# Kernel optimization log

Measured on AMD Instinct MI355X. Metric: run time of the kernel, lower is better.

The kernel has to match this reference:

```python
import jax, jax.numpy as jnp
import numpy as np

N_NODES = 20000
N_EDGES = 640000
B = 256
GNN_DIM = 256
HID = 512
INNER = 2048
RANK = 512
N_CLASSES = 3
N_GENES = 6640


def _ln(x, s, b, eps=1e-5):
    mu = jnp.mean(x, axis=-1, keepdims=True)
    var = jnp.mean(jnp.square(x - mu), axis=-1, keepdims=True)
    return (x - mu) * jax.lax.rsqrt(var + eps) * s + b


def setup_inputs() -> dict:
    key = jax.random.key(0)
    ks = jax.random.split(key, 16)
    s = 0.02
    return {
        "node_indices": jax.random.randint(ks[0], (B,), 0, N_NODES, dtype=jnp.int32),
        "edge_index": jax.random.randint(ks[1], (2, N_EDGES), 0, N_NODES, dtype=jnp.int32),
        "edge_weight": jax.random.uniform(ks[2], (N_EDGES,), dtype=jnp.float32),
        "partial_emb": jax.random.normal(ks[3], (N_NODES, GNN_DIM), dtype=jnp.float32),
        "oov_emb": jnp.zeros((1, GNN_DIM), jnp.float32),
        "gnn_ln_s": jnp.ones((3, GNN_DIM), jnp.float32),
        "gnn_ln_b": jnp.zeros((3, GNN_DIM), jnp.float32),
        "gnn_w": jax.random.normal(ks[4], (3, GNN_DIM, GNN_DIM), jnp.float32) * s,
        "gnn_b": jnp.zeros((3, GNN_DIM), jnp.float32),
        "post_w": jax.random.normal(ks[5], (GNN_DIM, GNN_DIM), jnp.float32) * s,
        "post_b": jnp.zeros((GNN_DIM,), jnp.float32),
        "pin_w": jax.random.normal(ks[6], (GNN_DIM, HID), jnp.float32) * s,
        "pin_b": jnp.zeros((HID,), jnp.float32),
        "blk_ln_s": jnp.ones((6, HID), jnp.float32),
        "blk_ln_b": jnp.zeros((6, HID), jnp.float32),
        "blk_w1": jax.random.normal(ks[7], (6, HID, INNER), jnp.float32) * s,
        "blk_b1": jnp.zeros((6, INNER), jnp.float32),
        "blk_w2": jax.random.normal(ks[8], (6, INNER, HID), jnp.float32) * s,
        "blk_b2": jnp.zeros((6, HID), jnp.float32),
        "pout_w": jax.random.normal(ks[9], (HID, N_CLASSES * RANK), jnp.float32) * s,
        "pout_b": jnp.zeros((N_CLASSES * RANK,), jnp.float32),
        "out_gene_emb": jax.random.normal(ks[10], (N_GENES, RANK), jnp.float32) * s,
    }


def reference(node_indices, edge_index, edge_weight, partial_emb, oov_emb,
              gnn_ln_s, gnn_ln_b, gnn_w, gnn_b, post_w, post_b,
              pin_w, pin_b, blk_ln_s, blk_ln_b, blk_w1, blk_b1, blk_w2, blk_b2,
              pout_w, pout_b, out_gene_emb):
    n = partial_emb.shape[0]
    src, dst = edge_index[0], edge_index[1]
    # --- trainable GNN tail: 3 layers of (LN -> weighted scatter-sum -> Linear -> ReLU) + residual ---
    x = partial_emb
    for i in range(3):
        h = _ln(x, gnn_ln_s[i], gnn_ln_b[i])
        msg = h[src] * edge_weight[:, None]              # [E, 256] gather (memory-bound)
        agg = jax.ops.segment_sum(msg, dst, num_segments=n)
        h = jax.nn.relu(agg @ gnn_w[i] + gnn_b[i])
        x = h + x
    x = x @ post_w + post_b                              # post_mp
    # --- OOV-safe perturbation embedding lookup ---
    oov = node_indices < 0
    safe = jnp.where(oov, 0, node_indices)
    pert = jnp.where(oov[:, None], oov_emb, x[safe])     # [B, 256]
    # --- bilinear head ---
    h = pert @ pin_w + pin_b
    for i in range(6):
        z = _ln(h, blk_ln_s[i], blk_ln_b[i])
        z = jax.nn.gelu(z @ blk_w1[i] + blk_b1[i], approximate=False)
        h = h + z @ blk_w2[i] + blk_b2[i]                # dropout = identity (eval)
    proj = (h @ pout_w + pout_b).reshape(h.shape[0], N_CLASSES, RANK)
    logits = jnp.einsum('bcr,gr->bcg', proj, out_gene_emb)
    return logits
```

## Files before the change

### kernel.cpp

```cpp
#include <hip/hip_runtime.h>
#include <hip/hip_bf16.h>
#include <math.h>

#define NNODES 20000
#define NEDGES 640000
#define BSZ 256
#define GDIM 256
#define HID 512
#define INNER 2048
#define RANK 512
#define NCLS 3
#define NGENES 6640

typedef __attribute__((ext_vector_type(8))) short bf16x8;
typedef __attribute__((ext_vector_type(4))) float f32x4;
typedef __attribute__((ext_vector_type(4))) unsigned u32x4;

__device__ inline float bf2f(unsigned short u) {
    return __uint_as_float(((unsigned)u) << 16);
}
__device__ inline unsigned short f2bf(float f) {
    unsigned u = __float_as_uint(f);
    u = u + 0x7fff + ((u >> 16) & 1);
    return (unsigned short)(u >> 16);
}
__device__ inline unsigned pk2(float a, float b) {
    return (unsigned)f2bf(a) | ((unsigned)f2bf(b) << 16);
}

__device__ inline u32x4 ld16_cg(const void* p) {
    u32x4 r;
    asm volatile("global_load_dwordx4 %0, %1, off sc0 sc1" : "=v"(r) : "v"(p) : "memory");
    return r;
}
__device__ inline void st4f_cg(void* p, float v) {
    asm volatile("global_store_dword %0, %1, off sc0 sc1" :: "v"(p), "v"(v) : "memory");
}
__device__ inline void st2_cg(void* p, unsigned short v) {
    unsigned w = v;
    asm volatile("global_store_short %0, %1, off sc0 sc1" :: "v"(p), "v"(w) : "memory");
}
__device__ inline void waitvm0(void) {
    asm volatile("s_waitcnt vmcnt(0)" ::: "memory");
    __builtin_amdgcn_sched_barrier(0);
}

__global__ void hist_k(const int* __restrict__ dst, int* __restrict__ counts, int E) {
    int e = blockIdx.x * 256 + threadIdx.x;
    if (e < E) atomicAdd(&counts[dst[e]], 1);
}

__global__ void scan1_k(const int* __restrict__ counts, int* __restrict__ incl,
                        int* __restrict__ bsums, int n) {
    __shared__ int s[256];
    int i = blockIdx.x * 256 + threadIdx.x;
    int v = (i < n) ? counts[i] : 0;
    s[threadIdx.x] = v;
    __syncthreads();
    for (int off = 1; off < 256; off <<= 1) {
        int t = (threadIdx.x >= off) ? s[threadIdx.x - off] : 0;
        __syncthreads();
        s[threadIdx.x] += t;
        __syncthreads();
    }
    if (i < n) incl[i] = s[threadIdx.x];
    if (threadIdx.x == 255) bsums[blockIdx.x] = s[255];
}

__global__ void scan2_k(const int* __restrict__ bsums, int* __restrict__ boffs, int nb) {
    __shared__ int s[128];
    int tid = threadIdx.x;
    int v = (tid < nb) ? bsums[tid] : 0;
    s[tid] = v;
    __syncthreads();
    for (int off = 1; off < 128; off <<= 1) {
        int t = (tid >= off) ? s[tid - off] : 0;
        __syncthreads();
        s[tid] += t;
        __syncthreads();
    }
    if (tid < nb) boffs[tid] = s[tid] - v;
}

__global__ void scan3_k(const int* __restrict__ incl, const int* __restrict__ counts,
                        const int* __restrict__ boffs, int* __restrict__ row_start,
                        int* __restrict__ cursor, int n) {
    int i = blockIdx.x * 256 + threadIdx.x;
    if (i < n) {
        int st = incl[i] - counts[i] + boffs[blockIdx.x];
        row_start[i] = st;
        cursor[i] = st;
    }
}

__global__ void scatter_k(const int* __restrict__ src, const int* __restrict__ dst,
                          const float* __restrict__ w, int* __restrict__ cursor,
                          int2* __restrict__ ep, int E) {
    int e = blockIdx.x * 256 + threadIdx.x;
    if (e < E) {
        int d = dst[e];
        int p = atomicAdd(&cursor[d], 1);
        ep[p] = make_int2(src[e], __float_as_int(w[e]));
    }
}

__global__ void flag_k(const int* __restrict__ idx, const int* __restrict__ row_start,
                       const int* __restrict__ counts, const int2* __restrict__ ep,
                       int* __restrict__ flag) {
    int r4 = blockIdx.x * 4 + (threadIdx.x >> 6);
    int lane = threadIdx.x & 63;
    int id = idx[r4];
    int row = id < 0 ? 0 : id;
    if (lane == 0) flag[row] = 1;
    int beg = row_start[row], cnt = counts[row];
    for (int t = lane; t < cnt; t += 64) flag[ep[beg + t].x] = 1;
}

__global__ void convall_k(const float* __restrict__ gnn_w, const float* __restrict__ post_w,
                          const float* __restrict__ pin_w, const float* __restrict__ blk_w1,
                          const float* __restrict__ blk_w2, const float* __restrict__ pout_w,
                          const float* __restrict__ gene, unsigned short* __restrict__ gnnT,
                          unsigned short* __restrict__ postT, unsigned short* __restrict__ pinT,
                          unsigned short* __restrict__ w1T, unsigned short* __restrict__ w2T,
                          unsigned short* __restrict__ poutT,
                          unsigned short* __restrict__ geneb) {
    int b = blockIdx.x;
    if (b >= 13440) {
        int t = b - 13440;
        const float4* xp = (const float4*)gene;
        int i = t * 512 + threadIdx.x * 2;
        float4 a = xp[i], c = xp[i + 1];
        *(ushort4*)(geneb + (size_t)i * 4) =
            make_ushort4(f2bf(a.x), f2bf(a.y), f2bf(a.z), f2bf(a.w));
        *(ushort4*)(geneb + (size_t)i * 4 + 4) =
            make_ushort4(f2bf(c.x), f2bf(c.y), f2bf(c.z), f2bf(c.w));
        return;
    }
    const float* W;
    unsigned short* WT;
    int K, N, tile;
    if (b < 192) {
        int l = b >> 6;
        tile = b & 63;
        W = gnn_w + (size_t)l * GDIM * GDIM;
        WT = gnnT + (size_t)l * GDIM * GDIM;
        K = GDIM; N = GDIM;
    } else if (b < 256) {
        tile = b - 192; W = post_w; WT = postT; K = GDIM; N = GDIM;
    } else if (b < 384) {
        tile = b - 256; W = pin_w; WT = pinT; K = GDIM; N = HID;
    } else if (b < 6528) {
        int t = b - 384;
        int l = t >> 10;
        tile = t & 1023;
        W = blk_w1 + (size_t)l * HID * INNER;
        WT = w1T + (size_t)l * INNER * HID;
        K = HID; N = INNER;
    } else if (b < 12672) {
        int t = b - 6528;
        int l = t >> 10;
        tile = t & 1023;
        W = blk_w2 + (size_t)l * INNER * HID;
        WT = w2T + (size_t)l * HID * INNER;
        K = INNER; N = HID;
    } else {
        tile = b - 12672; W = pout_w; WT = poutT; K = HID; N = NCLS * RANK;
    }
    __shared__ float s[32][33];
    int ntx = N >> 5;
    int k0 = (tile / ntx) << 5;
    int n0 = (tile % ntx) << 5;
    int tx = threadIdx.x & 31, ty = threadIdx.x >> 5;
#pragma unroll
    for (int i = 0; i < 4; i++)
        s[ty + 8 * i][tx] = W[(size_t)(k0 + ty + 8 * i) * N + n0 + tx];
    __syncthreads();
#pragma unroll
    for (int i = 0; i < 4; i++)
        WT[(size_t)(n0 + ty + 8 * i) * K + k0 + tx] = f2bf(s[tx][ty + 8 * i]);
}

template <bool FLAGGED>
__global__ void lnb_k(const float* __restrict__ X, const float* __restrict__ sc,
                      const float* __restrict__ bi, unsigned short* __restrict__ Y, int M,
                      const int* __restrict__ flag) {
    int row = blockIdx.x * 4 + (threadIdx.x >> 6);
    int lane = threadIdx.x & 63;
    if (row >= M) return;
    if (FLAGGED && !flag[row]) return;
    float4 v = ((const float4*)(X + (size_t)row * GDIM))[lane];
    float sum = v.x + v.y + v.z + v.w;
#pragma unroll
    for (int off = 32; off >= 1; off >>= 1) sum += __shfl_xor(sum, off);
    float mu = sum / GDIM;
    float a = v.x - mu, b = v.y - mu, c = v.z - mu, d = v.w - mu;
    float sq = a * a + b * b + c * c + d * d;
#pragma unroll
    for (int off = 32; off >= 1; off >>= 1) sq += __shfl_xor(sq, off);
    float rstd = rsqrtf(sq / GDIM + 1e-5f);
    float4 s4 = ((const float4*)sc)[lane];
    float4 b4 = ((const float4*)bi)[lane];
    *(ushort4*)(Y + (size_t)row * GDIM + lane * 4) =
        make_ushort4(f2bf(a * rstd * s4.x + b4.x), f2bf(b * rstd * s4.y + b4.y),
                     f2bf(c * rstd * s4.z + b4.z), f2bf(d * rstd * s4.w + b4.w));
}

__device__ inline void agg_row(int beg, int cnt, int lane, const int2* __restrict__ ep,
                               const unsigned short* __restrict__ H, float& a0, float& a1,
                               float& a2, float& a3) {
    int t = 0;
    for (; t + 16 <= cnt; t += 16) {
        int2 e[16];
#pragma unroll
        for (int u = 0; u < 16; u++) e[u] = ep[beg + t + u];
        ushort4 v[16];
#pragma unroll
        for (int u = 0; u < 16; u++)
            v[u] = *(const ushort4*)(H + (size_t)e[u].x * GDIM + lane * 4);
#pragma unroll
        for (int u = 0; u < 16; u++) {
            float w = __int_as_float(e[u].y);
            a0 = fmaf(bf2f(v[u].x), w, a0);
            a1 = fmaf(bf2f(v[u].y), w, a1);
            a2 = fmaf(bf2f(v[u].z), w, a2);
            a3 = fmaf(bf2f(v[u].w), w, a3);
        }
    }
    for (; t + 4 <= cnt; t += 4) {
        int2 e[4];
#pragma unroll
        for (int u = 0; u < 4; u++) e[u] = ep[beg + t + u];
        ushort4 v[4];
#pragma unroll
        for (int u = 0; u < 4; u++)
            v[u] = *(const ushort4*)(H + (size_t)e[u].x * GDIM + lane * 4);
#pragma unroll
        for (int u = 0; u < 4; u++) {
            float w = __int_as_float(e[u].y);
            a0 = fmaf(bf2f(v[u].x), w, a0);
            a1 = fmaf(bf2f(v[u].y), w, a1);
            a2 = fmaf(bf2f(v[u].z), w, a2);
            a3 = fmaf(bf2f(v[u].w), w, a3);
        }
    }
    for (; t < cnt; t++) {
        int2 e = ep[beg + t];
        float w = __int_as_float(e.y);
        ushort4 v = *(const ushort4*)(H + (size_t)e.x * GDIM + lane * 4);
        a0 = fmaf(bf2f(v.x), w, a0);
        a1 = fmaf(bf2f(v.y), w, a1);
        a2 = fmaf(bf2f(v.z), w, a2);
        a3 = fmaf(bf2f(v.w), w, a3);
    }
}

template <bool FLAGGED>
__global__ void aggb_k(const int* __restrict__ row_start, const int* __restrict__ counts,
                       const int2* __restrict__ ep, const unsigned short* __restrict__ H,
                       unsigned short* __restrict__ AGG, int n, const int* __restrict__ flag) {
    int row = blockIdx.x * 4 + (threadIdx.x >> 6);
    int lane = threadIdx.x & 63;
    if (row >= n) return;
    if (FLAGGED && !flag[row]) return;
    float a0 = 0.f, a1 = 0.f, a2 = 0.f, a3 = 0.f;
    agg_row(row_start[row], counts[row], lane, ep, H, a0, a1, a2, a3);
    *(ushort4*)(AGG + (size_t)row * GDIM + lane * 4) =
        make_ushort4(f2bf(a0), f2bf(a1), f2bf(a2), f2bf(a3));
}

__global__ void aggsel_k(const int* __restrict__ idx, const int* __restrict__ row_start,
                         const int* __restrict__ counts, const int2* __restrict__ ep,
                         const unsigned short* __restrict__ H, unsigned short* __restrict__ AGG) {
    int b = blockIdx.x * 4 + (threadIdx.x >> 6);
    int lane = threadIdx.x & 63;
    int id = idx[b];
    int row = id < 0 ? 0 : id;
    float a0 = 0.f, a1 = 0.f, a2 = 0.f, a3 = 0.f;
    agg_row(row_start[row], counts[row], lane, ep, H, a0, a1, a2, a3);
    *(ushort4*)(AGG + (size_t)b * GDIM + lane * 4) =
        make_ushort4(f2bf(a0), f2bf(a1), f2bf(a2), f2bf(a3));
}

template <int ACT, bool RES, bool BIAS>
__global__ __launch_bounds__(256) void mgemm_k(const unsigned short* __restrict__ A,
                                               const unsigned short* __restrict__ BT,
                                               const float* __restrict__ bias,
                                               const float* __restrict__ R,
                                               float* __restrict__ C, int M, int N, int K) {
    __shared__ unsigned short As[128 * 32];
    __shared__ unsigned short Bs[128 * 32];
    int m0 = blockIdx.y * 128, n0 = blockIdx.x * 128;
    int tid = threadIdx.x;
    int wave = tid >> 6, lane = tid & 63;
    int wm = (wave >> 1) * 64, wn = (wave & 1) * 64;
    int lrow = lane & 15, lq = lane >> 4;

    f32x4 acc[4][4];
    const f32x4 zz = {0.f, 0.f, 0.f, 0.f};
#pragma unroll
    for (int i = 0; i < 4; i++)
#pragma unroll
        for (int j = 0; j < 4; j++) acc[i][j] = zz;

    int r0 = tid >> 2;
    int q = tid & 3;

    for (int k0 = 0; k0 < K; k0 += 32) {
#pragma unroll
        for (int p = 0; p < 2; p++) {
            int row = r0 + p * 64;
            int gm = m0 + row;
            uint4 va = make_uint4(0, 0, 0, 0);
            if (gm < M) va = *(const uint4*)(A + (size_t)gm * K + k0 + q * 8);
            *(uint4*)&As[row * 32 + q * 8] = va;
            int gn = n0 + row;
            uint4 vb = make_uint4(0, 0, 0, 0);
            if (gn < N) vb = *(const uint4*)(BT + (size_t)gn * K + k0 + q * 8);
            *(uint4*)&Bs[row * 32 + q * 8] = vb;
        }
        __syncthreads();
        bf16x8 af[4], bf[4];
#pragma unroll
        for (int i = 0; i < 4; i++)
            af[i] = *(const bf16x8*)&As[(wm + i * 16 + lrow) * 32 + lq * 8];
#pragma unroll
        for (int j = 0; j < 4; j++)
            bf[j] = *(const bf16x8*)&Bs[(wn + j * 16 + lrow) * 32 + lq * 8];
#pragma unroll
        for (int i = 0; i < 4; i++)
#pragma unroll
            for (int j = 0; j < 4; j++)
                acc[i][j] =
                    __builtin_amdgcn_mfma_f32_16x16x32_bf16(af[i], bf[j], acc[i][j], 0, 0, 0);
        __syncthreads();
    }

#pragma unroll
    for (int i = 0; i < 4; i++) {
#pragma unroll
        for (int j = 0; j < 4; j++) {
            int gn = n0 + wn + j * 16 + lrow;
            if (gn >= N) continue;
            float bv = BIAS ? bias[gn] : 0.f;
#pragma unroll
            for (int r = 0; r < 4; r++) {
                int gm = m0 + wm + i * 16 + lq * 4 + r;
                if (gm >= M) continue;
                float v = acc[i][j][r] + bv;
                if (ACT == 1) v = fmaxf(v, 0.f);
                if (RES) v += R[(size_t)gm * N + gn];
                C[(size_t)gm * N + gn] = v;
            }
        }
    }
}

template <int ACT, int EPI>
__global__ __launch_bounds__(256) void mfull_k(const unsigned short* __restrict__ A,
                                               const unsigned short* __restrict__ BT,
                                               const float* __restrict__ bias,
                                               const int* __restrict__ idx,
                                               const float* __restrict__ aux,
                                               unsigned short* __restrict__ O, int M, int N,
                                               int K) {
    __shared__ unsigned short As[64 * 32];
    __shared__ unsigned short Bs[64 * 32];
    int m0 = blockIdx.y * 64, n0 = blockIdx.x * 64;
    int tid = threadIdx.x;
    int wave = tid >> 6, lane = tid & 63;
    int wm = wave * 16;
    int lrow = lane & 15, lq = lane >> 4;
    f32x4 acc[4];
    const f32x4 zz = {0.f, 0.f, 0.f, 0.f};
#pragma unroll
    for (int j = 0; j < 4; j++) acc[j] = zz;
    int r0 = tid >> 2;
    int q = tid & 3;
    for (int k0 = 0; k0 < K; k0 += 32) {
        *(uint4*)&As[r0 * 32 + q * 8] = *(const uint4*)(A + (size_t)(m0 + r0) * K + k0 + q * 8);
        *(uint4*)&Bs[r0 * 32 + q * 8] = *(const uint4*)(BT + (size_t)(n0 + r0) * K + k0 + q * 8);
        __syncthreads();
        bf16x8 af = *(const bf16x8*)&As[(wm + lrow) * 32 + lq * 8];
#pragma unroll
        for (int j = 0; j < 4; j++) {
            bf16x8 bfr = *(const bf16x8*)&Bs[(j * 16 + lrow) * 32 + lq * 8];
            acc[j] = __builtin_amdgcn_mfma_f32_16x16x32_bf16(af, bfr, acc[j], 0, 0, 0);
        }
        __syncthreads();
    }
#pragma unroll
    for (int j = 0; j < 4; j++) {
        int gn = n0 + j * 16 + lrow;
        float bv = bias[gn];
#pragma unroll
        for (int r = 0; r < 4; r++) {
            int gm = m0 + wm + lq * 4 + r;
            float v = acc[j][r] + bv;
            if (ACT == 1) v = fmaxf(v, 0.f);
            if (ACT == 2) v = 0.5f * v * (1.f + erff(v * 0.70710678118654752f));
            if (EPI == 2) {
                int id = idx[gm];
                int safe = id < 0 ? 0 : id;
                v += aux[(size_t)safe * N + gn];
            }
            if (EPI == 1) {
                if (idx[gm] < 0) v = aux[gn];
            }
            O[(size_t)gm * N + gn] = f2bf(v);
        }
    }
}


#define HGRID 256
#define LDPA 520
#define GBLK 32

__device__ inline void gsync_arrive(int* bar) {
    waitvm0();
    __syncthreads();
    if (threadIdx.x == 0)
        __hip_atomic_fetch_add(bar, 1, __ATOMIC_RELAXED, __HIP_MEMORY_SCOPE_AGENT);
}
__device__ inline void gsync_wait(int* bar, int target) {
    if (threadIdx.x == 0) {
        while (__hip_atomic_load(bar, __ATOMIC_RELAXED, __HIP_MEMORY_SCOPE_AGENT) < target)
            __builtin_amdgcn_s_sleep(2);
    }
    __builtin_amdgcn_s_barrier();
}

template <int ROWS, int KC, bool CG>
__device__ inline void stage_issue(const unsigned short* src, int ld, u32x4* regs) {
    constexpr int NL = ROWS * KC / 8 / 256;
    int tid = threadIdx.x;
#pragma unroll
    for (int it = 0; it < NL; it++) {
        int unit = it * 256 + tid;
        int row = unit / (KC / 8);
        int ucol = unit % (KC / 8);
        const unsigned short* p = src + (size_t)row * ld + ucol * 8;
        if (CG) regs[it] = ld16_cg(p);
        else regs[it] = *(const u32x4*)p;
    }
}
template <int ROWS, int KC>
__device__ inline void stage_write(unsigned short* dst, const u32x4* regs) {
    constexpr int NL = ROWS * KC / 8 / 256;
    int tid = threadIdx.x;
#pragma unroll
    for (int it = 0; it < NL; it++) {
        int unit = it * 256 + tid;
        int row = unit / (KC / 8);
        int ucol = unit % (KC / 8);
        *(u32x4*)&dst[row * LDPA + ucol * 8] = regs[it];
    }
}

template <int KC>
__device__ inline void mma_all(const unsigned short* As, const unsigned short* Bs, f32x4 acc[2]) {
    int tid = threadIdx.x, wave = tid >> 6, lane = tid & 63;
    int wm = (wave >> 1) * 16, wn = (wave & 1) * 32;
    int lrow = lane & 15, lq = lane >> 4;
#pragma unroll
    for (int kk = 0; kk < KC / 32; kk++) {
        bf16x8 af = *(const bf16x8*)&As[(wm + lrow) * LDPA + kk * 32 + lq * 8];
#pragma unroll
        for (int j = 0; j < 2; j++) {
            bf16x8 bfr = *(const bf16x8*)&Bs[(wn + j * 16 + lrow) * LDPA + kk * 32 + lq * 8];
            acc[j] = __builtin_amdgcn_mfma_f32_16x16x32_bf16(af, bfr, acc[j], 0, 0, 0);
        }
    }
}

__global__ __launch_bounds__(256) void head_k(
    const unsigned short* __restrict__ pertbf, const unsigned short* __restrict__ pinT,
    const float* __restrict__ pin_b, const float* __restrict__ blk_ln_s,
    const float* __restrict__ blk_ln_b, const unsigned short* __restrict__ w1T,
    const float* __restrict__ blk_b1, const unsigned short* __restrict__ w2T,
    const float* __restrict__ blk_b2, const unsigned short* __restrict__ poutT,
    const float* __restrict__ pout_b, float* __restrict__ hbuf,
    unsigned short* __restrict__ z1bf, unsigned short* __restrict__ projb,
    int* __restrict__ bar) {
    __shared__ unsigned short As[32 * LDPA];
    __shared__ unsigned short Bs[64 * LDPA];
    int b = blockIdx.x;
    int g = b >> 5;
    int t = b & 31;
    int* gbar = bar + g * 32;
    int m0 = g * 32;
    int tid = threadIdx.x;
    int wave = tid >> 6, lane = tid & 63;
    int wm = (wave >> 1) * 16, wn = (wave & 1) * 32;
    int lrow = lane & 15, lq = lane >> 4;
    int ph = 0;
    f32x4 acc[2];
    const f32x4 zz = {0.f, 0.f, 0.f, 0.f};
    u32x4 pf[16];

    if (t < 8) {
        int n0 = t * 64;
        u32x4 wreg[8], areg[4];
        stage_issue<64, 256, false>(pinT + (size_t)n0 * GDIM, GDIM, wreg);
        stage_issue<32, 256, false>(pertbf + (size_t)m0 * GDIM, GDIM, areg);
        waitvm0();
        stage_write<64, 256>(Bs, wreg);
        stage_write<32, 256>(As, areg);
        __syncthreads();
        acc[0] = zz; acc[1] = zz;
        mma_all<256>(As, Bs, acc);
#pragma unroll
        for (int j = 0; j < 2; j++) {
            int gn = n0 + wn + j * 16 + lrow;
            float bv = pin_b[gn];
#pragma unroll
            for (int r = 0; r < 4; r++) {
                int gm = m0 + wm + lq * 4 + r;
                st4f_cg(hbuf + (size_t)gm * HID + gn, acc[j][r] + bv);
            }
        }
    }
    gsync_arrive(gbar);
    stage_issue<64, 512, false>(w1T + (size_t)t * 64 * HID, HID, pf);
    gsync_wait(gbar, ++ph * GBLK);

    for (int i = 0; i < 6; i++) {
        {
            int n0 = t * 64;
            u32x4 hreg[16];
#pragma unroll
            for (int rr = 0; rr < 8; rr++) {
                const float* p = hbuf + (size_t)(m0 + wave * 8 + rr) * HID + lane * 8;
                hreg[2 * rr] = ld16_cg(p);
                hreg[2 * rr + 1] = ld16_cg(p + 4);
            }
            stage_write<64, 512>(Bs, pf);
            waitvm0();
            const float* ls = blk_ln_s + (size_t)i * HID;
            const float* lb = blk_ln_b + (size_t)i * HID;
            float4 s0 = ((const float4*)ls)[lane * 2], s1 = ((const float4*)ls)[lane * 2 + 1];
            float4 t0 = ((const float4*)lb)[lane * 2], t1 = ((const float4*)lb)[lane * 2 + 1];
#pragma unroll
            for (int rr = 0; rr < 8; rr++) {
                float f0 = __uint_as_float(hreg[2 * rr][0]);
                float f1 = __uint_as_float(hreg[2 * rr][1]);
                float f2 = __uint_as_float(hreg[2 * rr][2]);
                float f3 = __uint_as_float(hreg[2 * rr][3]);
                float f4 = __uint_as_float(hreg[2 * rr + 1][0]);
                float f5 = __uint_as_float(hreg[2 * rr + 1][1]);
                float f6 = __uint_as_float(hreg[2 * rr + 1][2]);
                float f7 = __uint_as_float(hreg[2 * rr + 1][3]);
                float sum = f0 + f1 + f2 + f3 + f4 + f5 + f6 + f7;
#pragma unroll
                for (int off = 32; off >= 1; off >>= 1) sum += __shfl_xor(sum, off);
                float mu = sum * (1.f / HID);
                float d0 = f0 - mu, d1 = f1 - mu, d2 = f2 - mu, d3 = f3 - mu;
                float d4 = f4 - mu, d5 = f5 - mu, d6 = f6 - mu, d7 = f7 - mu;
                float sq = d0 * d0 + d1 * d1 + d2 * d2 + d3 * d3 + d4 * d4 + d5 * d5 +
                           d6 * d6 + d7 * d7;
#pragma unroll
                for (int off = 32; off >= 1; off >>= 1) sq += __shfl_xor(sq, off);
                float rstd = rsqrtf(sq * (1.f / HID) + 1e-5f);
                u32x4 pk;
                pk[0] = pk2(d0 * rstd * s0.x + t0.x, d1 * rstd * s0.y + t0.y);
                pk[1] = pk2(d2 * rstd * s0.z + t0.z, d3 * rstd * s0.w + t0.w);
                pk[2] = pk2(d4 * rstd * s1.x + t1.x, d5 * rstd * s1.y + t1.y);
                pk[3] = pk2(d6 * rstd * s1.z + t1.z, d7 * rstd * s1.w + t1.w);
                *(u32x4*)&As[(wave * 8 + rr) * LDPA + lane * 8] = pk;
            }
            __syncthreads();
            acc[0] = zz; acc[1] = zz;
            mma_all<512>(As, Bs, acc);
#pragma unroll
            for (int j = 0; j < 2; j++) {
                int gn = n0 + wn + j * 16 + lrow;
                float bv = blk_b1[(size_t)i * INNER + gn];
#pragma unroll
                for (int r = 0; r < 4; r++) {
                    int gm = m0 + wm + lq * 4 + r;
                    float v = acc[j][r] + bv;
                    v = 0.5f * v * (1.f + erff(v * 0.70710678118654752f));
                    st2_cg(z1bf + (size_t)gm * INNER + gn, f2bf(v));
                }
            }
        }
        gsync_arrive(gbar);
        stage_issue<64, 512, false>(
// ... 49 lines not shown
            float a = __uint_as_float(areg[it][0]), c = __uint_as_float(areg[it][1]);
            float d = __uint_as_float(areg[it][2]), e = __uint_as_float(areg[it][3]);
            uint2 w2v;
            w2v.x = pk2(a, c);
            w2v.y = pk2(d, e);
            *(uint2*)&As[row * LDPA + ucol * 4] = w2v;
        }
        __syncthreads();
        acc[0] = zz; acc[1] = zz;
        mma_all<512>(As, Bs, acc);
#pragma unroll
        for (int j = 0; j < 2; j++) {
            int gn = n0 + wn + j * 16 + lrow;
            float bv = pout_b[gn];
#pragma unroll
            for (int r = 0; r < 4; r++) {
                int gm = m0 + wm + lq * 4 + r;
                projb[(size_t)gm * (NCLS * RANK) + gn] = f2bf(acc[j][r] + bv);
            }
        }
    }
}

extern "C" void kernel_launch(void* const* d_in, const int* in_sizes, int n_in,
                              void* d_out, int out_size, void* d_ws, size_t ws_size,
                              hipStream_t stream) {
    const int* node_indices = (const int*)d_in[0];
    const int* edge_src = (const int*)d_in[1];
    const int* edge_dst = edge_src + NEDGES;
    const float* edge_w = (const float*)d_in[2];
    const float* partial_emb = (const float*)d_in[3];
    const float* oov_emb = (const float*)d_in[4];
    const float* gnn_ln_s = (const float*)d_in[5];
    const float* gnn_ln_b = (const float*)d_in[6];
    const float* gnn_w = (const float*)d_in[7];
    const float* gnn_b = (const float*)d_in[8];
    const float* post_w = (const float*)d_in[9];
    const float* post_b = (const float*)d_in[10];
    const float* pin_w = (const float*)d_in[11];
    const float* pin_b = (const float*)d_in[12];
    const float* blk_ln_s = (const float*)d_in[13];
    const float* blk_ln_b = (const float*)d_in[14];
    const float* blk_w1 = (const float*)d_in[15];
    const float* blk_b1 = (const float*)d_in[16];
    const float* blk_w2 = (const float*)d_in[17];
    const float* blk_b2 = (const float*)d_in[18];
    const float* pout_w = (const float*)d_in[19];
    const float* pout_b = (const float*)d_in[20];
    const float* gene = (const float*)d_in[21];
    float* out = (float*)d_out;

    char* p = (char*)d_ws;
    auto alloc = [&](size_t bytes) {
        char* r = p;
        p += (bytes + 255) & ~(size_t)255;
        return r;
    };
    int* counts = (int*)alloc(NNODES * 4);
    int* incl = (int*)alloc(NNODES * 4);
    int* bsums = (int*)alloc(128 * 4);
    int* boffs = (int*)alloc(128 * 4);
    int* row_start = (int*)alloc(NNODES * 4);
    int* cursor = (int*)alloc(NNODES * 4);
    int* flag = (int*)alloc(NNODES * 4);
    int2* epack = (int2*)alloc((size_t)NEDGES * 8);
    float* part = (float*)alloc((size_t)NNODES * GDIM * 4);
    unsigned short* ln_bf = (unsigned short*)part;
    unsigned short* aggbf = (unsigned short*)((char*)part + (size_t)NNODES * GDIM * 2);
    float* xa = (float*)alloc((size_t)NNODES * GDIM * 4);
    float* xb = (float*)alloc((size_t)NNODES * GDIM * 4);
    float* hbuf = (float*)alloc((size_t)BSZ * HID * 4);
    unsigned short* aggselb = (unsigned short*)alloc((size_t)BSZ * GDIM * 2);
    unsigned short* pertinbf = (unsigned short*)alloc((size_t)BSZ * GDIM * 2);
    unsigned short* pertbf = (unsigned short*)alloc((size_t)BSZ * GDIM * 2);
    unsigned short* z1bf = (unsigned short*)alloc((size_t)BSZ * INNER * 2);
    unsigned short* projb = (unsigned short*)alloc((size_t)BSZ * NCLS * RANK * 2);
    unsigned short* gnnT = (unsigned short*)alloc((size_t)3 * GDIM * GDIM * 2);
    unsigned short* postT = (unsigned short*)alloc((size_t)GDIM * GDIM * 2);
    unsigned short* pinT = (unsigned short*)alloc((size_t)HID * GDIM * 2);
    unsigned short* w1T = (unsigned short*)alloc((size_t)6 * INNER * HID * 2);
    unsigned short* w2T = (unsigned short*)alloc((size_t)6 * HID * INNER * 2);
    unsigned short* poutT = (unsigned short*)alloc((size_t)NCLS * RANK * HID * 2);
    unsigned short* geneb = (unsigned short*)alloc((size_t)NGENES * RANK * 2);
    int* bar = (int*)alloc(1024);

    const int EB = (NEDGES + 255) / 256;
    const int NB = (NNODES + 255) / 256;

    convall_k<<<15100, 256, 0, stream>>>(gnn_w, post_w, pin_w, blk_w1, blk_w2, pout_w, gene,
                                         gnnT, postT, pinT, w1T, w2T, poutT, geneb);

    (void)hipMemsetAsync(counts, 0, NNODES * 4, stream);
    (void)hipMemsetAsync(flag, 0, NNODES * 4, stream);
    (void)hipMemsetAsync(bar, 0, 1024, stream);
    hist_k<<<EB, 256, 0, stream>>>(edge_dst, counts, NEDGES);
    scan1_k<<<NB, 256, 0, stream>>>(counts, incl, bsums, NNODES);
    scan2_k<<<1, 128, 0, stream>>>(bsums, boffs, NB);
    scan3_k<<<NB, 256, 0, stream>>>(incl, counts, boffs, row_start, cursor, NNODES);
    scatter_k<<<EB, 256, 0, stream>>>(edge_src, edge_dst, edge_w, cursor, epack, NEDGES);
    flag_k<<<BSZ / 4, 256, 0, stream>>>(node_indices, row_start, counts, epack, flag);

    const float* x_in = partial_emb;
    float* bufs[2] = {xa, xb};
    for (int i = 0; i < 2; i++) {
        lnb_k<false><<<(NNODES + 3) / 4, 256, 0, stream>>>(
            x_in, gnn_ln_s + i * GDIM, gnn_ln_b + i * GDIM, ln_bf, NNODES, nullptr);
        if (i == 0)
            aggb_k<false><<<(NNODES + 3) / 4, 256, 0, stream>>>(row_start, counts, epack, ln_bf,
                                                                aggbf, NNODES, nullptr);
        else
            aggb_k<true><<<(NNODES + 3) / 4, 256, 0, stream>>>(row_start, counts, epack, ln_bf,
                                                               aggbf, NNODES, flag);
        float* x_out = bufs[i];
        mgemm_k<1, true, true><<<dim3(GDIM / 128, (NNODES + 127) / 128), 256, 0, stream>>>(
            aggbf, gnnT + (size_t)i * GDIM * GDIM, gnn_b + i * GDIM, x_in, x_out, NNODES, GDIM,
            GDIM);
        x_in = x_out;
    }
    lnb_k<true><<<(NNODES + 3) / 4, 256, 0, stream>>>(xb, gnn_ln_s + 2 * GDIM,
                                                      gnn_ln_b + 2 * GDIM, ln_bf, NNODES, flag);
    aggsel_k<<<BSZ / 4, 256, 0, stream>>>(node_indices, row_start, counts, epack, ln_bf, aggselb);
    mfull_k<1, 2><<<dim3(GDIM / 64, BSZ / 64), 256, 0, stream>>>(
        aggselb, gnnT + (size_t)2 * GDIM * GDIM, gnn_b + 2 * GDIM, node_indices, xb, pertinbf,
        BSZ, GDIM, GDIM);

    mfull_k<0, 1><<<dim3(GDIM / 64, BSZ / 64), 256, 0, stream>>>(
        pertinbf, postT, post_b, node_indices, oov_emb, pertbf, BSZ, GDIM, GDIM);

    head_k<<<HGRID, 256, 0, stream>>>(pertbf, pinT, pin_b, blk_ln_s, blk_ln_b, w1T, blk_b1, w2T,
                                      blk_b2, poutT, pout_b, hbuf, z1bf, projb, bar);

    mgemm_k<0, false, false><<<dim3((NGENES + 127) / 128, (BSZ * NCLS) / 128), 256, 0, stream>>>(
        projb, geneb, nullptr, nullptr, out, BSZ * NCLS, NGENES, RANK);
}
```

Baseline: 514.8 us.

## Fuse CSR build, weight conversion and tail GEMMs into persistent grid-synced kernels

Replaces the memsets, histogram, three scan kernels, scatter, flag marking, weight transposition and first LayerNorm with a single persistent 256-block kernel that uses atomic-counter grid barriers between phases. The selected-row aggregation and the third GNN layer plus post-MP GEMMs are moved into the head kernel as extra grid-synced phases. The aim is to remove many kernel launches and their gaps. In exchange, each phase is limited to 256 blocks, and the spin barriers assume every block is co-resident on the device.

```diff
diff --git a/kernel.cpp b/kernel.cpp
--- a/kernel.cpp
+++ b/kernel.cpp
@@ -15,6 +15,7 @@
 typedef __attribute__((ext_vector_type(8))) short bf16x8;
 typedef __attribute__((ext_vector_type(4))) float f32x4;
 typedef __attribute__((ext_vector_type(4))) unsigned u32x4;
+typedef __attribute__((ext_vector_type(2))) unsigned u32x2;
 
 __device__ inline float bf2f(unsigned short u) {
     return __uint_as_float(((unsigned)u) << 16);
@@ -33,8 +34,24 @@
     asm volatile("global_load_dwordx4 %0, %1, off sc0 sc1" : "=v"(r) : "v"(p) : "memory");
     return r;
 }
+__device__ inline u32x2 ld8_cg(const void* p) {
+    u32x2 r;
+    asm volatile("global_load_dwordx2 %0, %1, off sc0 sc1" : "=v"(r) : "v"(p) : "memory");
+    return r;
+}
+__device__ inline int ld4i_cg(const int* p) {
+    int r;
+    asm volatile("global_load_dword %0, %1, off sc0 sc1" : "=v"(r) : "v"(p) : "memory");
+    return r;
+}
 __device__ inline void st4f_cg(void* p, float v) {
     asm volatile("global_store_dword %0, %1, off sc0 sc1" :: "v"(p), "v"(v) : "memory");
+}
+__device__ inline void st4i_cg(int* p, int v) {
+    asm volatile("global_store_dword %0, %1, off sc0 sc1" :: "v"(p), "v"(v) : "memory");
+}
+__device__ inline void st8_cg(void* p, u32x2 v) {
+    asm volatile("global_store_dwordx2 %0, %1, off sc0 sc1" :: "v"(p), "v"(v) : "memory");
 }
 __device__ inline void st2_cg(void* p, unsigned short v) {
     unsigned w = v;
@@ -45,139 +62,191 @@
     __builtin_amdgcn_sched_barrier(0);
 }
 
-__global__ void hist_k(const int* __restrict__ dst, int* __restrict__ counts, int E) {
-    int e = blockIdx.x * 256 + threadIdx.x;
-    if (e < E) atomicAdd(&counts[dst[e]], 1);
-}
-
-__global__ void scan1_k(const int* __restrict__ counts, int* __restrict__ incl,
-                        int* __restrict__ bsums, int n) {
+__device__ inline void gsync_arrive(int* bar) {
+    waitvm0();
+    __syncthreads();
+    if (threadIdx.x == 0)
+        __hip_atomic_fetch_add(bar, 1, __ATOMIC_RELAXED, __HIP_MEMORY_SCOPE_AGENT);
+}
+__device__ inline void gsync_wait(int* bar, int target) {
+    if (threadIdx.x == 0) {
+        while (__hip_atomic_load(bar, __ATOMIC_RELAXED, __HIP_MEMORY_SCOPE_AGENT) < target)
+            __builtin_amdgcn_s_sleep(2);
+    }
+    __builtin_amdgcn_s_barrier();
+}
+__device__ inline void gsync_c(int* bar, int target) {
+    gsync_arrive(bar);
+    gsync_wait(bar, target);
+}
+
+__global__ __launch_bounds__(256) void csr_k(
+    const int* __restrict__ edge_src, const int* __restrict__ edge_dst,
+    const float* __restrict__ edge_w, const int* __restrict__ node_indices,
+    const float* __restrict__ partial_emb, const float* __restrict__ gnn_ln_s,
+    const float* __restrict__ gnn_ln_b, unsigned short* __restrict__ ln_bf,
+    int* __restrict__ counts, int* __restrict__ incl, int* __restrict__ bsums,
+    int* __restrict__ boffs, int* __restrict__ row_start, int* __restrict__ cursor,
+    int* __restrict__ flag, int2* __restrict__ ep, const float* __restrict__ gnn_w,
+    const float* __restrict__ post_w, const float* __restrict__ pin_w,
+    const float* __restrict__ blk_w1, const float* __restrict__ blk_w2,
+    const float* __restrict__ pout_w, const float* __restrict__ gene,
+    unsigned short* __restrict__ gnnT, unsigned short* __restrict__ postT,
+    unsigned short* __restrict__ pinT, unsigned short* __restrict__ w1T,
+    unsigned short* __restrict__ w2T, unsigned short* __restrict__ poutT,
+    unsigned short* __restrict__ geneb, int* __restrict__ gbar) {
     __shared__ int s[256];
-    int i = blockIdx.x * 256 + threadIdx.x;
-    int v = (i < n) ? counts[i] : 0;
-    s[threadIdx.x] = v;
-    __syncthreads();
-    for (int off = 1; off < 256; off <<= 1) {
-        int t = (threadIdx.x >= off) ? s[threadIdx.x - off] : 0;
-        __syncthreads();
-        s[threadIdx.x] += t;
-        __syncthreads();
-    }
-    if (i < n) incl[i] = s[threadIdx.x];
-    if (threadIdx.x == 255) bsums[blockIdx.x] = s[255];
-}
-
-__global__ void scan2_k(const int* __restrict__ bsums, int* __restrict__ boffs, int nb) {
-    __shared__ int s[128];
-    int tid = threadIdx.x;
-    int v = (tid < nb) ? bsums[tid] : 0;
-    s[tid] = v;
-    __syncthreads();
-    for (int off = 1; off < 128; off <<= 1) {
-        int t = (tid >= off) ? s[tid - off] : 0;
-        __syncthreads();
-        s[tid] += t;
-        __syncthreads();
-    }
-    if (tid < nb) boffs[tid] = s[tid] - v;
-}
-
-__global__ void scan3_k(const int* __restrict__ incl, const int* __restrict__ counts,
-                        const int* __restrict__ boffs, int* __restrict__ row_start,
-                        int* __restrict__ cursor, int n) {
-    int i = blockIdx.x * 256 + threadIdx.x;
-    if (i < n) {
-        int st = incl[i] - counts[i] + boffs[blockIdx.x];
-        row_start[i] = st;
-        cursor[i] = st;
-    }
-}
-
-__global__ void scatter_k(const int* __restrict__ src, const int* __restrict__ dst,
-                          const float* __restrict__ w, int* __restrict__ cursor,
-                          int2* __restrict__ ep, int E) {
-    int e = blockIdx.x * 256 + threadIdx.x;
-    if (e < E) {
-        int d = dst[e];
+    __shared__ float sc[32][33];
+    const int b = blockIdx.x, tid = threadIdx.x;
+    const int gs = b * 256 + tid;
+    const int NB_ = (NNODES + 255) / 256;
+
+    for (int i = gs; i < NNODES; i += 65536) {
+        st4i_cg(counts + i, 0);
+        st4i_cg(flag + i, 0);
+    }
+    {
+        int lane = tid & 63;
+        float4 s4 = ((const float4*)gnn_ln_s)[lane];
+        float4 b4 = ((const float4*)gnn_ln_b)[lane];
+        for (int row = b * 4 + (tid >> 6); row < NNODES; row += 1024) {
+            float4 v = ((const float4*)(partial_emb + (size_t)row * GDIM))[lane];
+            float sum = v.x + v.y + v.z + v.w;
+#pragma unroll
+            for (int off = 32; off >= 1; off >>= 1) sum += __shfl_xor(sum, off);
+            float mu = sum / GDIM;
+            float a = v.x - mu, b2 = v.y - mu, c = v.z - mu, d = v.w - mu;
+            float sq = a * a + b2 * b2 + c * c + d * d;
+#pragma unroll
+            for (int off = 32; off >= 1; off >>= 1) sq += __shfl_xor(sq, off);
+            float rstd = rsqrtf(sq / GDIM + 1e-5f);
+            *(ushort4*)(ln_bf + (size_t)row * GDIM + lane * 4) =
+                make_ushort4(f2bf(a * rstd * s4.x + b4.x), f2bf(b2 * rstd * s4.y + b4.y),
+                             f2bf(c * rstd * s4.z + b4.z), f2bf(d * rstd * s4.w + b4.w));
+        }
+    }
+    gsync_c(gbar, 256);
+    for (int e = gs; e < NEDGES; e += 65536) atomicAdd(&counts[edge_dst[e]], 1);
+    gsync_c(gbar, 512);
+    if (b < NB_) {
+        int i = b * 256 + tid;
+        int v = 0;
+        if (i < NNODES) v = ld4i_cg(counts + i);
+        waitvm0();
+        s[tid] = v;
+        __syncthreads();
+        for (int off = 1; off < 256; off <<= 1) {
+            int t2 = (tid >= off) ? s[tid - off] : 0;
+            __syncthreads();
+            s[tid] += t2;
+            __syncthreads();
+        }
+        if (i < NNODES) st4i_cg(incl + i, s[tid]);
+        if (tid == 255) st4i_cg(bsums + b, s[255]);
+    }
+    gsync_c(gbar, 768);
+    if (b == 0) {
+        int v = 0;
+        if (tid < NB_) v = ld4i_cg(bsums + tid);
+        waitvm0();
+        s[tid] = v;
+        __syncthreads();
+        for (int off = 1; off < 256; off <<= 1) {
+            int t2 = (tid >= off) ? s[tid - off] : 0;
+            __syncthreads();
+            s[tid] += t2;
+            __syncthreads();
+        }
+        if (tid < NB_) st4i_cg(boffs + tid, s[tid] - v);
+    }
+    gsync_c(gbar, 1024);
+    for (int i = gs; i < NNODES; i += 65536) {
+        int a = ld4i_cg(incl + i);
+        int c = ld4i_cg(counts + i);
+        int o = ld4i_cg(boffs + (i >> 8));
+        waitvm0();
+        int st = a - c + o;
+        st4i_cg(row_start + i, st);
+        st4i_cg(cursor + i, st);
+    }
+    gsync_c(gbar, 1280);
+    for (int e = gs; e < NEDGES; e += 65536) {
+        int d = edge_dst[e];
         int p = atomicAdd(&cursor[d], 1);
-        ep[p] = make_int2(src[e], __float_as_int(w[e]));
-    }
-}
-
-__global__ void flag_k(const int* __restrict__ idx, const int* __restrict__ row_start,
-                       const int* __restrict__ counts, const int2* __restrict__ ep,
-                       int* __restrict__ flag) {
-    int r4 = blockIdx.x * 4 + (threadIdx.x >> 6);
-    int lane = threadIdx.x & 63;
-    int id = idx[r4];
-    int row = id < 0 ? 0 : id;
-    if (lane == 0) flag[row] = 1;
-    int beg = row_start[row], cnt = counts[row];
-    for (int t = lane; t < cnt; t += 64) flag[ep[beg + t].x] = 1;
-}
-
-__global__ void convall_k(const float* __restrict__ gnn_w, const float* __restrict__ post_w,
-                          const float* __restrict__ pin_w, const float* __restrict__ blk_w1,
-                          const float* __restrict__ blk_w2, const float* __restrict__ pout_w,
-                          const float* __restrict__ gene, unsigned short* __restrict__ gnnT,
-                          unsigned short* __restrict__ postT, unsigned short* __restrict__ pinT,
-                          unsigned short* __restrict__ w1T, unsigned short* __restrict__ w2T,
-                          unsigned short* __restrict__ poutT,
-                          unsigned short* __restrict__ geneb) {
-    int b = blockIdx.x;
-    if (b >= 13440) {
-        int t = b - 13440;
-        const float4* xp = (const float4*)gene;
-        int i = t * 512 + threadIdx.x * 2;
-        float4 a = xp[i], c = xp[i + 1];
-        *(ushort4*)(geneb + (size_t)i * 4) =
-            make_ushort4(f2bf(a.x), f2bf(a.y), f2bf(a.z), f2bf(a.w));
-        *(ushort4*)(geneb + (size_t)i * 4 + 4) =
-            make_ushort4(f2bf(c.x), f2bf(c.y), f2bf(c.z), f2bf(c.w));
-        return;
-    }
-    const float* W;
-    unsigned short* WT;
-    int K, N, tile;
-    if (b < 192) {
-        int l = b >> 6;
-        tile = b & 63;
-        W = gnn_w + (size_t)l * GDIM * GDIM;
-        WT = gnnT + (size_t)l * GDIM * GDIM;
-        K = GDIM; N = GDIM;
-    } else if (b < 256) {
-        tile = b - 192; W = post_w; WT = postT; K = GDIM; N = GDIM;
-    } else if (b < 384) {
-        tile = b - 256; W = pin_w; WT = pinT; K = GDIM; N = HID;
-    } else if (b < 6528) {
-        int t = b - 384;
-        int l = t >> 10;
-        tile = t & 1023;
-        W = blk_w1 + (size_t)l * HID * INNER;
-        WT = w1T + (size_t)l * INNER * HID;
-        K = HID; N = INNER;
-    } else if (b < 12672) {
-        int t = b - 6528;
-        int l = t >> 10;
-        tile = t & 1023;
-        W = blk_w2 + (size_t)l * INNER * HID;
-        WT = w2T + (size_t)l * HID * INNER;
-        K = INNER; N = HID;
-    } else {
-        tile = b - 12672; W = pout_w; WT = poutT; K = HID; N = NCLS * RANK;
-    }
-    __shared__ float s[32][33];
-    int ntx = N >> 5;
-    int k0 = (tile / ntx) << 5;
-    int n0 = (tile % ntx) << 5;
-    int tx = threadIdx.x & 31, ty = threadIdx.x >> 5;
-#pragma unroll
-    for (int i = 0; i < 4; i++)
-        s[ty + 8 * i][tx] = W[(size_t)(k0 + ty + 8 * i) * N + n0 + tx];
-    __syncthreads();
-#pragma unroll
-    for (int i = 0; i < 4; i++)
-        WT[(size_t)(n0 + ty + 8 * i) * K + k0 + tx] = f2bf(s[tx][ty + 8 * i]);
+        u32x2 pk;
+        pk[0] = (unsigned)edge_src[e];
+        pk[1] = __float_as_uint(edge_w[e]);
+        st8_cg(ep + p, pk);
+    }
+    gsync_c(gbar, 1536);
+    {
+        int id = node_indices[b];
+        int row = id < 0 ? 0 : id;
+        if (tid == 0) st4i_cg(flag + row, 1);
+        int beg = ld4i_cg(row_start + row);
+        int cnt = ld4i_cg(counts + row);
+        waitvm0();
+        for (int t2 = tid; t2 < cnt; t2 += 256) {
+            u32x2 e2 = ld8_cg(ep + beg + t2);
+            waitvm0();
+            st4i_cg(flag + (int)e2[0], 1);
+        }
+    }
+    for (int tb = b; tb < 15100; tb += 256) {
+        if (tb >= 13440) {
+            int t2 = tb - 13440;
+            const float4* xp = (const float4*)gene;
+            int i = t2 * 512 + tid * 2;
+            float4 a = xp[i], c = xp[i + 1];
+            *(ushort4*)(geneb + (size_t)i * 4) =
+                make_ushort4(f2bf(a.x), f2bf(a.y), f2bf(a.z), f2bf(a.w));
+            *(ushort4*)(geneb + (size_t)i * 4 + 4) =
+                make_ushort4(f2bf(c.x), f2bf(c.y), f2bf(c.z), f2bf(c.w));
+            continue;
+        }
+        const float* W;
+        unsigned short* WT;
+        int K, N, tile;
+        if (tb < 192) {
+            int l = tb >> 6;
+            tile = tb & 63;
+            W = gnn_w + (size_t)l * GDIM * GDIM;
+            WT = gnnT + (size_t)l * GDIM * GDIM;
+            K = GDIM; N = GDIM;
+        } else if (tb < 256) {
+            tile = tb - 192; W = post_w; WT = postT; K = GDIM; N = GDIM;
+        } else if (tb < 384) {
+            tile = tb - 256; W = pin_w; WT = pinT; K = GDIM; N = HID;
+        } else if (tb < 6528) {
+            int t2 = tb - 384;
+            int l = t2 >> 10;
+            tile = t2 & 1023;
+            W = blk_w1 + (size_t)l * HID * INNER;
+            WT = w1T + (size_t)l * INNER * HID;
+            K = HID; N = INNER;
+        } else if (tb < 12672) {
+            int t2 = tb - 6528;
+            int l = t2 >> 10;
+            tile = t2 & 1023;
+            W = blk_w2 + (size_t)l * INNER * HID;
+            WT = w2T + (size_t)l * HID * INNER;
+            K = INNER; N = HID;
+        } else {
+            tile = tb - 12672; W = pout_w; WT = poutT; K = HID; N = NCLS * RANK;
+        }
+        int ntx = N >> 5;
+        int k0 = (tile / ntx) << 5;
+        int n0 = (tile % ntx) << 5;
+        int tx = tid & 31, ty = tid >> 5;
+#pragma unroll
+        for (int i = 0; i < 4; i++)
+            sc[ty + 8 * i][tx] = W[(size_t)(k0 + ty + 8 * i) * N + n0 + tx];
+        __syncthreads();
+#pragma unroll
+        for (int i = 0; i < 4; i++)
+            WT[(size_t)(n0 + ty + 8 * i) * K + k0 + tx] = f2bf(sc[tx][ty + 8 * i]);
+        __syncthreads();
+    }
 }
 
 template <bool FLAGGED>
@@ -265,19 +334,6 @@
     float a0 = 0.f, a1 = 0.f, a2 = 0.f, a3 = 0.f;
     agg_row(row_start[row], counts[row], lane, ep, H, a0, a1, a2, a3);
     *(ushort4*)(AGG + (size_t)row * GDIM + lane * 4) =
-        make_ushort4(f2bf(a0), f2bf(a1), f2bf(a2), f2bf(a3));
-}
-
-__global__ void aggsel_k(const int* __restrict__ idx, const int* __restrict__ row_start,
-                         const int* __restrict__ counts, const int2* __restrict__ ep,
-                         const unsigned short* __restrict__ H, unsigned short* __restrict__ AGG) {
-    int b = blockIdx.x * 4 + (threadIdx.x >> 6);
-    int lane = threadIdx.x & 63;
-    int id = idx[b];
-    int row = id < 0 ? 0 : id;
-    float a0 = 0.f, a1 = 0.f, a2 = 0.f, a3 = 0.f;
-    agg_row(row_start[row], counts[row], lane, ep, H, a0, a1, a2, a3);
-    *(ushort4*)(AGG + (size_t)b * GDIM + lane * 4) =
         make_ushort4(f2bf(a0), f2bf(a1), f2bf(a2), f2bf(a3));
 }
 
@@ -355,80 +411,10 @@
     }
 }
 
-template <int ACT, int EPI>
-__global__ __launch_bounds__(256) void mfull_k(const unsigned short* __restrict__ A,
-                                               const unsigned short* __restrict__ BT,
-                                               const float* __restrict__ bias,
-                                               const int* __restrict__ idx,
-                                               const float* __restrict__ aux,
-                                               unsigned short* __restrict__ O, int M, int N,
-                                               int K) {
-    __shared__ unsigned short As[64 * 32];
-    __shared__ unsigned short Bs[64 * 32];
-    int m0 = blockIdx.y * 64, n0 = blockIdx.x * 64;
-    int tid = threadIdx.x;
-    int wave = tid >> 6, lane = tid & 63;
-    int wm = wave * 16;
-    int lrow = lane & 15, lq = lane >> 4;
-    f32x4 acc[4];
-    const f32x4 zz = {0.f, 0.f, 0.f, 0.f};
-#pragma unroll
-    for (int j = 0; j < 4; j++) acc[j] = zz;
-    int r0 = tid >> 2;
-    int q = tid & 3;
-    for (int k0 = 0; k0 < K; k0 += 32) {
-        *(uint4*)&As[r0 * 32 + q * 8] = *(const uint4*)(A + (size_t)(m0 + r0) * K + k0 + q * 8);
-        *(uint4*)&Bs[r0 * 32 + q * 8] = *(const uint4*)(BT + (size_t)(n0 + r0) * K + k0 + q * 8);
-        __syncthreads();
-        bf16x8 af = *(const bf16x8*)&As[(wm + lrow) * 32 + lq * 8];
-#pragma unroll
-        for (int j = 0; j < 4; j++) {
-            bf16x8 bfr = *(const bf16x8*)&Bs[(j * 16 + lrow) * 32 + lq * 8];
-            acc[j] = __builtin_amdgcn_mfma_f32_16x16x32_bf16(af, bfr, acc[j], 0, 0, 0);
-        }
-        __syncthreads();
-    }
-#pragma unroll
-    for (int j = 0; j < 4; j++) {
-        int gn = n0 + j * 16 + lrow;
-        float bv = bias[gn];
-#pragma unroll
-        for (int r = 0; r < 4; r++) {
-            int gm = m0 + wm + lq * 4 + r;
-            float v = acc[j][r] + bv;
-            if (ACT == 1) v = fmaxf(v, 0.f);
-            if (ACT == 2) v = 0.5f * v * (1.f + erff(v * 0.70710678118654752f));
-            if (EPI == 2) {
-                int id = idx[gm];
-                int safe = id < 0 ? 0 : id;
-                v += aux[(size_t)safe * N + gn];
-            }
-            if (EPI == 1) {
-                if (idx[gm] < 0) v = aux[gn];
-            }
-            O[(size_t)gm * N + gn] = f2bf(v);
-        }
-    }
-}
-
 
 #define HGRID 256
 #define LDPA 520
 #define GBLK 32
-
-__device__ inline void gsync_arrive(int* bar) {
-    waitvm0();
-    __syncthreads();
-    if (threadIdx.x == 0)
-        __hip_atomic_fetch_add(bar, 1, __ATOMIC_RELAXED, __HIP_MEMORY_SCOPE_AGENT);
-}
-__device__ inline void gsync_wait(int* bar, int target) {
-    if (threadIdx.x == 0) {
-        while (__hip_atomic_load(bar, __ATOMIC_RELAXED, __HIP_MEMORY_SCOPE_AGENT) < target)
-            __builtin_amdgcn_s_sleep(2);
-    }
-    __builtin_amdgcn_s_barrier();
-}
 
 template <int ROWS, int KC, bool CG>
 __device__ inline void stage_issue(const unsigned short* src, int ld, u32x4* regs) {
@@ -474,14 +460,20 @@
 }
 
 __global__ __launch_bounds__(256) void head_k(
-    const unsigned short* __restrict__ pertbf, const unsigned short* __restrict__ pinT,
-    const float* __restrict__ pin_b, const float* __restrict__ blk_ln_s,
-    const float* __restrict__ blk_ln_b, const unsigned short* __restrict__ w1T,
-    const float* __restrict__ blk_b1, const unsigned short* __restrict__ w2T,
-    const float* __restrict__ blk_b2, const unsigned short* __restrict__ poutT,
-    const float* __restrict__ pout_b, float* __restrict__ hbuf,
-    unsigned short* __restrict__ z1bf, unsigned short* __restrict__ projb,
-    int* __restrict__ bar) {
+    const int* __restrict__ node_indices, const int* __restrict__ row_start,
+    const int* __restrict__ counts, const int2* __restrict__ ep,
+    const unsigned short* __restrict__ lnbf, const unsigned short* __restrict__ gnnT3,
+    const float* __restrict__ gnnb3, const float* __restrict__ xb,
+    const unsigned short* __restrict__ postT, const float* __restrict__ post_b,
+    const float* __restrict__ oov_emb, unsigned short* __restrict__ aggselb,
+    unsigned short* __restrict__ pertinbf, unsigned short* __restrict__ pertbf,
+    const unsigned short* __restrict__ pinT, const float* __restrict__ pin_b,
+    const float* __restrict__ blk_ln_s, const float* __restrict__ blk_ln_b,
+    const unsigned short* __restrict__ w1T, const float* __restrict__ blk_b1,
+    const unsigned short* __restrict__ w2T, const float* __restrict__ blk_b2,
+    const unsigned short* __restrict__ poutT, const float* __restrict__ pout_b,
+    float* __restrict__ hbuf, unsigned short* __restrict__ z1bf,
+    unsigned short* __restrict__ projb, int* __restrict__ bar) {
     __shared__ unsigned short As[32 * LDPA];
     __shared__ unsigned short Bs[64 * LDPA];
     int b = blockIdx.x;
@@ -498,11 +490,103 @@
     const f32x4 zz = {0.f, 0.f, 0.f, 0.f};
     u32x4 pf[16];
 
+    {
+        int bb = m0 + t;
+        int id = node_indices[bb];
+        int row = id < 0 ? 0 : id;
+        int beg = row_start[row], cnt = counts[row];
+        float a0 = 0.f, a1 = 0.f, a2 = 0.f, a3 = 0.f;
+        for (int e2 = wave; e2 < cnt; e2 += 4) {
+            int2 ed = ep[beg + e2];
+            float w = __int_as_float(ed.y);
+            ushort4 v = *(const ushort4*)(lnbf + (size_t)ed.x * GDIM + lane * 4);
+            a0 = fmaf(bf2f(v.x), w, a0);
+            a1 = fmaf(bf2f(v.y), w, a1);
+            a2 = fmaf(bf2f(v.z), w, a2);
+            a3 = fmaf(bf2f(v.w), w, a3);
+        }
+        float* red = (float*)As;
+        red[wave * 256 + lane * 4 + 0] = a0;
+        red[wave * 256 + lane * 4 + 1] = a1;
+        red[wave * 256 + lane * 4 + 2] = a2;
+        red[wave * 256 + lane * 4 + 3] = a3;
+        __syncthreads();
+        if (wave == 0) {
+            float s0 = red[lane * 4] + red[256 + lane * 4] + red[512 + lane * 4] +
+                       red[768 + lane * 4];
+            float s1 = red[lane * 4 + 1] + red[256 + lane * 4 + 1] + red[512 + lane * 4 + 1] +
+                       red[768 + lane * 4 + 1];
+            float s2 = red[lane * 4 + 2] + red[256 + lane * 4 + 2] + red[512 + lane * 4 + 2] +
+                       red[768 + lane * 4 + 2];
+            float s3 = red[lane * 4 + 3] + red[256 + lane * 4 + 3] + red[512 + lane * 4 + 3] +
+                       red[768 + lane * 4 + 3];
+            u32x2 pk;
+            pk[0] = pk2(s0, s1);
+            pk[1] = pk2(s2, s3);
+            st8_cg(aggselb + (size_t)bb * GDIM + lane * 4, pk);
+        }
+    }
+    gsync_c(gbar, ++ph * GBLK);
+
+    if (t < 4) {
+        int n0 = t * 64;
+        u32x4 wreg[8], areg[4];
+        stage_issue<64, 256, false>(gnnT3 + (size_t)n0 * GDIM, GDIM, wreg);
+        stage_issue<32, 256, true>(aggselb + (size_t)m0 * GDIM, GDIM, areg);
+        waitvm0();
+        stage_write<64, 256>(Bs, wreg);
+        stage_write<32, 256>(As, areg);
+        __syncthreads();
+        acc[0] = zz; acc[1] = zz;
+        mma_all<256>(As, Bs, acc);
+#pragma unroll
+        for (int j = 0; j < 2; j++) {
+            int gn = n0 + wn + j * 16 + lrow;
+            float bv = gnnb3[gn];
+#pragma unroll
+            for (int r = 0; r < 4; r++) {
+                int gmb = m0 + wm + lq * 4 + r;
+                float v = fmaxf(acc[j][r] + bv, 0.f);
+                int id = node_indices[gmb];
+                int safe = id < 0 ? 0 : id;
+                v += xb[(size_t)safe * GDIM + gn];
+                st2_cg(pertinbf + (size_t)gmb * GDIM + gn, f2bf(v));
+            }
+        }
+    }
+    gsync_c(gbar, ++ph * GBLK);
+
+    if (t < 4) {
+        int n0 = t * 64;
+        u32x4 wreg[8], areg[4];
+        stage_issue<64, 256, false>(postT + (size_t)n0 * GDIM, GDIM, wreg);
+        stage_issue<32, 256, true>(pertinbf + (size_t)m0 * GDIM, GDIM, areg);
+        waitvm0();
+        stage_write<64, 256>(Bs, wreg);
+        stage_write<32, 256>(As, areg);
+        __syncthreads();
+        acc[0] = zz; acc[1] = zz;
+        mma_all<256>(As, Bs, acc);
+#pragma unroll
+        for (int j = 0; j < 2; j++) {
+            int gn = n0 + wn + j * 16 + lrow;
+            float bv = post_b[gn];
+#pragma unroll
+            for (int r = 0; r < 4; r++) {
+                int gmb = m0 + wm + lq * 4 + r;
+                float v = acc[j][r] + bv;
+                if (node_indices[gmb] < 0) v = oov_emb[gn];
+                st2_cg(pertbf + (size_t)gmb * GDIM + gn, f2bf(v));
+            }
+        }
+    }
+    gsync_c(gbar, ++ph * GBLK);
+
     if (t < 8) {
         int n0 = t * 64;
         u32x4 wreg[8], areg[4];
         stage_issue<64, 256, false>(pinT + (size_t)n0 * GDIM, GDIM, wreg);
-        stage_issue<32, 256, false>(pertbf + (size_t)m0 * GDIM, GDIM, areg);
+        stage_issue<32, 256, true>(pertbf + (size_t)m0 * GDIM, GDIM, areg);
         waitvm0();
         stage_write<64, 256>(Bs, wreg);
         stage_write<32, 256>(As, areg);
@@ -718,53 +802,34 @@
     unsigned short* w2T = (unsigned short*)alloc((size_t)6 * HID * INNER * 2);
     unsigned short* poutT = (unsigned short*)alloc((size_t)NCLS * RANK * HID * 2);
     unsigned short* geneb = (unsigned short*)alloc((size_t)NGENES * RANK * 2);
-    int* bar = (int*)alloc(1024);
-
-    const int EB = (NEDGES + 255) / 256;
-    const int NB = (NNODES + 255) / 256;
-
-    convall_k<<<15100, 256, 0, stream>>>(gnn_w, post_w, pin_w, blk_w1, blk_w2, pout_w, gene,
-                                         gnnT, postT, pinT, w1T, w2T, poutT, geneb);
-
-    (void)hipMemsetAsync(counts, 0, NNODES * 4, stream);
-    (void)hipMemsetAsync(flag, 0, NNODES * 4, stream);
-    (void)hipMemsetAsync(bar, 0, 1024, stream);
-    hist_k<<<EB, 256, 0, stream>>>(edge_dst, counts, NEDGES);
-    scan1_k<<<NB, 256, 0, stream>>>(counts, incl, bsums, NNODES);
-    scan2_k<<<1, 128, 0, stream>>>(bsums, boffs, NB);
-    scan3_k<<<NB, 256, 0, stream>>>(incl, counts, boffs, row_start, cursor, NNODES);
-    scatter_k<<<EB, 256, 0, stream>>>(edge_src, edge_dst, edge_w, cursor, epack, NEDGES);
-    flag_k<<<BSZ / 4, 256, 0, stream>>>(node_indices, row_start, counts, epack, flag);
-
-    const float* x_in = partial_emb;
-    float* bufs[2] = {xa, xb};
-    for (int i = 0; i < 2; i++) {
-        lnb_k<false><<<(NNODES + 3) / 4, 256, 0, stream>>>(
-            x_in, gnn_ln_s + i * GDIM, gnn_ln_b + i * GDIM, ln_bf, NNODES, nullptr);
-        if (i == 0)
-            aggb_k<false><<<(NNODES + 3) / 4, 256, 0, stream>>>(row_start, counts, epack, ln_bf,
-                                                                aggbf, NNODES, nullptr);
-        else
-            aggb_k<true><<<(NNODES + 3) / 4, 256, 0, stream>>>(row_start, counts, epack, ln_bf,
-                                                               aggbf, NNODES, flag);
-        float* x_out = bufs[i];
-        mgemm_k<1, true, true><<<dim3(GDIM / 128, (NNODES + 127) / 128), 256, 0, stream>>>(
-            aggbf, gnnT + (size_t)i * GDIM * GDIM, gnn_b + i * GDIM, x_in, x_out, NNODES, GDIM,
-            GDIM);
-        x_in = x_out;
-    }
+    int* bar = (int*)alloc(2048);
+
+    (void)hipMemsetAsync(bar, 0, 2048, stream);
+
+    csr_k<<<256, 256, 0, stream>>>(edge_src, edge_dst, edge_w, node_indices, partial_emb,
+                                   gnn_ln_s, gnn_ln_b, ln_bf, counts, incl, bsums, boffs,
+                                   row_start, cursor, flag, epack, gnn_w, post_w, pin_w, blk_w1,
+                                   blk_w2, pout_w, gene, gnnT, postT, pinT, w1T, w2T, poutT,
+                                   geneb, bar + 256);
+
+    aggb_k<false><<<(NNODES + 3) / 4, 256, 0, stream>>>(row_start, counts, epack, ln_bf, aggbf,
+                                                        NNODES, nullptr);
+    mgemm_k<1, true, true><<<dim3(GDIM / 128, (NNODES + 127) / 128), 256, 0, stream>>>(
+        aggbf, gnnT, gnn_b, partial_emb, xa, NNODES, GDIM, GDIM);
+    lnb_k<false><<<(NNODES + 3) / 4, 256, 0, stream>>>(xa, gnn_ln_s + GDIM, gnn_ln_b + GDIM,
+                                                       ln_bf, NNODES, nullptr);
+    aggb_k<true><<<(NNODES + 3) / 4, 256, 0, stream>>>(row_start, counts, epack, ln_bf, aggbf,
+                                                       NNODES, flag);
+    mgemm_k<1, true, true><<<dim3(GDIM / 128, (NNODES + 127) / 128), 256, 0, stream>>>(
+        aggbf, gnnT + (size_t)GDIM * GDIM, gnn_b + GDIM, xa, xb, NNODES, GDIM, GDIM);
     lnb_k<true><<<(NNODES + 3) / 4, 256, 0, stream>>>(xb, gnn_ln_s + 2 * GDIM,
                                                       gnn_ln_b + 2 * GDIM, ln_bf, NNODES, flag);
-    aggsel_k<<<BSZ / 4, 256, 0, stream>>>(node_indices, row_start, counts, epack, ln_bf, aggselb);
-    mfull_k<1, 2><<<dim3(GDIM / 64, BSZ / 64), 256, 0, stream>>>(
-        aggselb, gnnT + (size_t)2 * GDIM * GDIM, gnn_b + 2 * GDIM, node_indices, xb, pertinbf,
-        BSZ, GDIM, GDIM);
-
-    mfull_k<0, 1><<<dim3(GDIM / 64, BSZ / 64), 256, 0, stream>>>(
-        pertinbf, postT, post_b, node_indices, oov_emb, pertbf, BSZ, GDIM, GDIM);
-
-    head_k<<<HGRID, 256, 0, stream>>>(pertbf, pinT, pin_b, blk_ln_s, blk_ln_b, w1T, blk_b1, w2T,
-                                      blk_b2, poutT, pout_b, hbuf, z1bf, projb, bar);
+
+    head_k<<<HGRID, 256, 0, stream>>>(node_indices, row_start, counts, epack, ln_bf,
+                                      gnnT + (size_t)2 * GDIM * GDIM, gnn_b + 2 * GDIM, xb,
+                                      postT, post_b, oov_emb, aggselb, pertinbf, pertbf, pinT,
+                                      pin_b, blk_ln_s, blk_ln_b, w1T, blk_b1, w2T, blk_b2,
+                                      poutT, pout_b, hbuf, z1bf, projb, bar);
 
     mgemm_k<0, false, false><<<dim3((NGENES + 127) / 128, (BSZ * NCLS) / 128), 256, 0, stream>>>(
         projb, geneb, nullptr, nullptr, out, BSZ * NCLS, NGENES, RANK);
```

Measured after the change: 604.9 us. +17.5%, slower.
